# Performance work log

Measured on AMD Instinct MI355X. Metric: run time of the kernel, lower is better.

Reference implementation:

```python
import jax, jax.numpy as jnp
import numpy as np

N = 50000          # total atoms in batch
E = 1_600_000      # total edges (flattened neighbor list)
ELEM = 64          # elem_fea_len
NBR = 32           # nbr_fea_len
EPS = 1e-5         # BatchNorm eps


def _batchnorm(x, gamma, beta):
    # training-mode BatchNorm1d: per-feature batch stats (biased variance)
    mean = x.mean(axis=0)
    var = ((x - mean) ** 2).mean(axis=0)
    return gamma * (x - mean) * jax.lax.rsqrt(var + EPS) + beta


def setup_inputs() -> dict:
    key = jax.random.key(0)
    ks = jax.random.split(key, 6)
    atom_in_fea = jax.random.normal(ks[0], (N, ELEM), jnp.float32)
    nbr_fea = jax.random.normal(ks[1], (E, NBR), jnp.float32)
    self_fea_idx = jnp.sort(jax.random.randint(ks[2], (E,), 0, N))
    nbr_fea_idx = jax.random.randint(ks[3], (E,), 0, N)
    fan_in = 2 * ELEM + NBR
    W = jax.random.normal(ks[4], (fan_in, 2 * ELEM), jnp.float32) * (1.0 / np.sqrt(fan_in))
    b = jnp.zeros((2 * ELEM,), jnp.float32)
    gamma1 = jnp.ones((2 * ELEM,), jnp.float32)
    beta1 = jnp.zeros((2 * ELEM,), jnp.float32)
    gamma2 = jnp.ones((ELEM,), jnp.float32)
    beta2 = jnp.zeros((ELEM,), jnp.float32)
    return {
        "atom_in_fea": atom_in_fea,
        "nbr_fea": nbr_fea,
        "self_fea_idx": self_fea_idx,
        "nbr_fea_idx": nbr_fea_idx,
        "W": W,
        "b": b,
        "gamma1": gamma1,
        "beta1": beta1,
        "gamma2": gamma2,
        "beta2": beta2,
    }


def reference(atom_in_fea, nbr_fea, self_fea_idx, nbr_fea_idx,
              W, b, gamma1, beta1, gamma2, beta2):
    # gather + concat: (E, 2*ELEM + NBR)
    total_fea = jnp.concatenate(
        [atom_in_fea[self_fea_idx], atom_in_fea[nbr_fea_idx], nbr_fea], axis=1)
    total_fea = total_fea @ W + b                    # fc_full: (E, 2*ELEM)
    total_fea = _batchnorm(total_fea, gamma1, beta1)  # bn1
    filter_fea, core_fea = jnp.split(total_fea, 2, axis=1)
    nbr_msg = jax.nn.sigmoid(filter_fea) * jax.nn.softplus(core_fea)  # (E, ELEM)
    nbr_sumed = jax.ops.segment_sum(nbr_msg, self_fea_idx, num_segments=N)
    nbr_sumed = _batchnorm(nbr_sumed, gamma2, beta2)  # bn2
    return jax.nn.softplus(atom_in_fea + nbr_sumed)   # residual + softplus2
```

## Files before the change

kernel.cpp:

```cpp
#include <hip/hip_runtime.h>

#define E_TOT 1600000
#define N_AT  50000

typedef unsigned short u16;
typedef __attribute__((ext_vector_type(8))) __bf16 bf16x8;
typedef __attribute__((ext_vector_type(4))) float f32x4;

__device__ __forceinline__ u16 f2bf(float f) {
    unsigned int u = __float_as_uint(f);
    return (u16)((u + 0x7FFFu + ((u >> 16) & 1u)) >> 16);
}
__device__ __forceinline__ float softplus_f(float x) {
    return fmaxf(x, 0.0f) + __logf(1.0f + __expf(-fabsf(x)));
}
__device__ __forceinline__ bf16x8 cvt8(const float* __restrict__ p) {
    f32x4 a = *(const f32x4*)p;
    f32x4 b = *(const f32x4*)(p + 4);
    bf16x8 r;
    r[0] = (__bf16)a[0]; r[1] = (__bf16)a[1]; r[2] = (__bf16)a[2]; r[3] = (__bf16)a[3];
    r[4] = (__bf16)b[0]; r[5] = (__bf16)b[1]; r[6] = (__bf16)b[2]; r[7] = (__bf16)b[3];
    return r;
}

__global__ __launch_bounds__(256) void k_pre(const float* __restrict__ atom,
                                             u16* __restrict__ ab) {
    int i = blockIdx.x * 256 + threadIdx.x;
    ab[i] = f2bf(atom[i]);
}

__global__ __launch_bounds__(256) void k0_swizzle_w(const float* __restrict__ W,
                                                    u16* __restrict__ wf) {
    int t = blockIdx.x * 256 + threadIdx.x;
    if (t >= 5 * 8 * 64 * 8) return;
    int j = t & 7;
    int lane = (t >> 3) & 63;
    int ct = (t >> 9) & 7;
    int kt = t >> 12;
    int k = kt * 32 + (lane >> 4) * 8 + j;
    int c = ct * 16 + (lane & 15);
    wf[t] = f2bf(W[k * 128 + c]);
}

__device__ __forceinline__ void gemm_tile(const u16* __restrict__ ab,
                                          const float* __restrict__ nbr,
                                          const int* __restrict__ sidx,
                                          const int* __restrict__ nidx,
                                          const u16* __restrict__ wf,
                                          int rb, int lane, f32x4 acc[2][8]) {
    const int mrow = lane & 15, quad = lane >> 4;
    const int r0 = rb + mrow, r1 = r0 + 16;
    const int s0 = sidx[r0], s1 = sidx[r1];
    const int n0 = nidx[r0], n1 = nidx[r1];

    const u16* pa00 = ab + s0 * 64 + quad * 8;
    const u16* pa02 = ab + n0 * 64 + quad * 8;
    const u16* pa10 = ab + s1 * 64 + quad * 8;
    const u16* pa12 = ab + n1 * 64 + quad * 8;

    bf16x8 A0[5], A1[5];
    A0[0] = *(const bf16x8*)pa00;        A1[0] = *(const bf16x8*)pa10;
    A0[1] = *(const bf16x8*)(pa00 + 32); A1[1] = *(const bf16x8*)(pa10 + 32);
    A0[2] = *(const bf16x8*)pa02;        A1[2] = *(const bf16x8*)pa12;
    A0[3] = *(const bf16x8*)(pa02 + 32); A1[3] = *(const bf16x8*)(pa12 + 32);
    A0[4] = cvt8(nbr + r0 * 32 + quad * 8);
    A1[4] = cvt8(nbr + r1 * 32 + quad * 8);

#pragma unroll
    for (int kt = 0; kt < 5; kt++) {
#pragma unroll
        for (int ct = 0; ct < 8; ct++) {
            bf16x8 b = *(const bf16x8*)(wf + ((kt * 8 + ct) * 64 + lane) * 8);
            acc[0][ct] = __builtin_amdgcn_mfma_f32_16x16x32_bf16(A0[kt], b, acc[0][ct], 0, 0, 0);
            acc[1][ct] = __builtin_amdgcn_mfma_f32_16x16x32_bf16(A1[kt], b, acc[1][ct], 0, 0, 0);
        }
    }
}

__global__ __launch_bounds__(256) void k1_stats(const u16* __restrict__ ab,
                                                const float* __restrict__ nbr,
                                                const int* __restrict__ sidx,
                                                const int* __restrict__ nidx,
                                                const u16* __restrict__ wf,
                                                float* __restrict__ statsbuf) {
    const int tx = threadIdx.x, lane = tx & 63, w = tx >> 6;
    const int rb = blockIdx.x * 128 + w * 32;

    f32x4 acc[2][8];
#pragma unroll
    for (int i = 0; i < 2; i++)
#pragma unroll
        for (int j = 0; j < 8; j++) { f32x4 z = {0.f, 0.f, 0.f, 0.f}; acc[i][j] = z; }

    gemm_tile(ab, nbr, sidx, nidx, wf, rb, lane, acc);

    __shared__ float bs[256];
    bs[tx] = 0.0f;
    __syncthreads();

    const int mrow = lane & 15, quad = lane >> 4;
#pragma unroll
    for (int ct = 0; ct < 8; ct++) {
        float s = 0.f, q = 0.f;
#pragma unroll
        for (int rf = 0; rf < 2; rf++)
#pragma unroll
            for (int rg = 0; rg < 4; rg++) {
                float v = acc[rf][ct][rg];
                s += v; q += v * v;
            }
        s += __shfl_xor(s, 16, 64); s += __shfl_xor(s, 32, 64);
        q += __shfl_xor(q, 16, 64); q += __shfl_xor(q, 32, 64);
        if (quad == 0) {
            atomicAdd(&bs[ct * 16 + mrow], s);
            atomicAdd(&bs[128 + ct * 16 + mrow], q);
        }
    }
    __syncthreads();
    statsbuf[blockIdx.x * 256 + tx] = bs[tx];
}

__global__ __launch_bounds__(256) void k2_reduce(const float* __restrict__ statsbuf,
                                                 float* __restrict__ sums1) {
    const int tx = threadIdx.x;
    float s = 0.f;
    for (int b = blockIdx.x; b < 12500; b += gridDim.x)
        s += statsbuf[b * 256 + tx];
    atomicAdd(&sums1[tx], s);
}

__global__ __launch_bounds__(256) void k3_msg(const u16* __restrict__ ab,
                                              const float* __restrict__ nbr,
                                              const int* __restrict__ sidx,
                                              const int* __restrict__ nidx,
                                              const u16* __restrict__ wf,
                                              const float* __restrict__ sums1,
                                              const float* __restrict__ g1,
                                              const float* __restrict__ b1,
                                              float* __restrict__ ns) {
    const int tx = threadIdx.x, lane = tx & 63, w = tx >> 6;
    const int blk = blockIdx.x;
    const int rb = blk * 128 + w * 32;

    f32x4 acc[2][8];
#pragma unroll
    for (int i = 0; i < 2; i++)
#pragma unroll
        for (int j = 0; j < 8; j++) { f32x4 z = {0.f, 0.f, 0.f, 0.f}; acc[i][j] = z; }

    gemm_tile(ab, nbr, sidx, nidx, wf, rb, lane, acc);

    __shared__ float msg[128][66];
    const int mrow = lane & 15, quad = lane >> 4;
    const float invE = 1.0f / (float)E_TOT;

#pragma unroll
    for (int ct = 0; ct < 4; ct++) {
        const int cf = ct * 16 + mrow;
        const int cc = cf + 64;
        float mf = sums1[cf] * invE;
        float vf = sums1[128 + cf] * invE - mf * mf;
        float af = g1[cf] * rsqrtf(vf + 1e-5f);
        float kf = b1[cf] - af * mf;
        float mc = sums1[cc] * invE;
        float vc = sums1[128 + cc] * invE - mc * mc;
        float ac = g1[cc] * rsqrtf(vc + 1e-5f);
        float kc = b1[cc] - ac * mc;
#pragma unroll
        for (int rf = 0; rf < 2; rf++)
#pragma unroll
            for (int rg = 0; rg < 4; rg++) {
                float xf = af * acc[rf][ct][rg] + kf;
                float xc = ac * acc[rf][ct + 4][rg] + kc;
                float sg = 1.0f / (1.0f + __expf(-xf));
                msg[w * 32 + rf * 16 + quad * 4 + rg][cf] = sg * softplus_f(xc);
            }
    }
    __syncthreads();

    const int ebase = blk * 128 + w * 32;
    float accum = 0.f;
    int cur = sidx[ebase];
    for (int i = 0; i < 32; i++) {
        int idx = sidx[ebase + i];
        if (idx != cur) {
            atomicAdd(&ns[cur * 64 + lane], accum);
            accum = 0.f;
            cur = idx;
        }
        accum += msg[w * 32 + i][lane];
    }
    atomicAdd(&ns[cur * 64 + lane], accum);
}

__global__ __launch_bounds__(256) void k4_bn2stats(const float* __restrict__ ns,
                                                   float* __restrict__ sums2) {
    const int tx = threadIdx.x;
    const int col = tx & 63, rg = tx >> 6;
    float s = 0.f, q = 0.f;
    for (int r = blockIdx.x * 4 + rg; r < N_AT; r += 256 * 4) {
        float v = ns[r * 64 + col];
        s += v; q += v * v;
    }
    atomicAdd(&sums2[col], s);
    atomicAdd(&sums2[64 + col], q);
}

__global__ __launch_bounds__(256) void k5_final(const float* __restrict__ atom,
                                                const float* __restrict__ ns,
                                                const float* __restrict__ sums2,
                                                const float* __restrict__ g2,
                                                const float* __restrict__ b2,
                                                float* __restrict__ out) {
    const int i = blockIdx.x * 256 + threadIdx.x;
    const int col = i & 63;
    const float invN = 1.0f / (float)N_AT;
    float mean = sums2[col] * invN;
    float var = sums2[64 + col] * invN - mean * mean;
    float a2 = g2[col] * rsqrtf(var + 1e-5f);
    float c2 = b2[col] - a2 * mean;
    float x = atom[i] + a2 * ns[i] + c2;
    out[i] = softplus_f(x);
}

extern "C" void kernel_launch(void* const* d_in, const int* in_sizes, int n_in,
                              void* d_out, int out_size, void* d_ws, size_t ws_size,
                              hipStream_t stream) {
    const float* atom = (const float*)d_in[0];
    const float* nbr  = (const float*)d_in[1];
    const int* sidx   = (const int*)d_in[2];
    const int* nidx   = (const int*)d_in[3];
    const float* W    = (const float*)d_in[4];
    const float* g1   = (const float*)d_in[6];
    const float* b1   = (const float*)d_in[7];
    const float* g2   = (const float*)d_in[8];
    const float* b2   = (const float*)d_in[9];
    float* out = (float*)d_out;

    char* ws = (char*)d_ws;
    const size_t STAT1_OFF = 0;
    const size_t SUM1_OFF  = STAT1_OFF + (size_t)12500 * 256 * 4;
    const size_t NS_OFF    = SUM1_OFF + 1024;
    const size_t SUM2_OFF  = NS_OFF + (size_t)N_AT * 64 * 4;
    const size_t WF_OFF    = SUM2_OFF + 512;
    const size_t AB_OFF    = WF_OFF + 40960;

    float* statsbuf = (float*)(ws + STAT1_OFF);
    float* sums1    = (float*)(ws + SUM1_OFF);
    float* nsumed   = (float*)(ws + NS_OFF);
    float* sums2    = (float*)(ws + SUM2_OFF);
    u16*   wf       = (u16*)(ws + WF_OFF);
    u16*   ab       = (u16*)(ws + AB_OFF);

    hipMemsetAsync(ws + SUM1_OFF, 0, 1024 + (size_t)N_AT * 64 * 4 + 512, stream);

    k_pre<<<(N_AT * 64) / 256, 256, 0, stream>>>(atom, ab);
    k0_swizzle_w<<<80, 256, 0, stream>>>(W, wf);
    k1_stats<<<E_TOT / 128, 256, 0, stream>>>(ab, nbr, sidx, nidx, wf, statsbuf);
    k2_reduce<<<64, 256, 0, stream>>>(statsbuf, sums1);
    k3_msg<<<E_TOT / 128, 256, 0, stream>>>(ab, nbr, sidx, nidx, wf, sums1, g1, b1, nsumed);
    k4_bn2stats<<<256, 256, 0, stream>>>(nsumed, sums2);
    k5_final<<<(N_AT * 64) / 256, 256, 0, stream>>>(atom, nsumed, sums2, g2, b2, out);
}
```

Measured before the change: 803.6 us.

## Fuse setup kernels, stage weights in LDS, cache bf16 nbr features, double tile rows

```diff
diff --git a/kernel.cpp b/kernel.cpp
--- a/kernel.cpp
+++ b/kernel.cpp
@@ -7,6 +7,14 @@
 typedef __attribute__((ext_vector_type(8))) __bf16 bf16x8;
 typedef __attribute__((ext_vector_type(4))) float f32x4;
 
+#define SUM1_OFF 0
+#define SUM2_OFF 1024
+#define WF_OFF   2048
+#define NS_OFF   43008
+#define AB_OFF   12843008
+#define NBRB_OFF 19243008
+#define WS_FULL  121643008ULL
+
 __device__ __forceinline__ u16 f2bf(float f) {
     unsigned int u = __float_as_uint(f);
     return (u16)((u + 0x7FFFu + ((u >> 16) & 1u)) >> 16);
@@ -14,101 +22,128 @@
 __device__ __forceinline__ float softplus_f(float x) {
     return fmaxf(x, 0.0f) + __logf(1.0f + __expf(-fabsf(x)));
 }
-__device__ __forceinline__ bf16x8 cvt8(const float* __restrict__ p) {
-    f32x4 a = *(const f32x4*)p;
-    f32x4 b = *(const f32x4*)(p + 4);
+__device__ __forceinline__ bf16x8 cvt8v(f32x4 a, f32x4 b) {
     bf16x8 r;
     r[0] = (__bf16)a[0]; r[1] = (__bf16)a[1]; r[2] = (__bf16)a[2]; r[3] = (__bf16)a[3];
     r[4] = (__bf16)b[0]; r[5] = (__bf16)b[1]; r[6] = (__bf16)b[2]; r[7] = (__bf16)b[3];
     return r;
 }
 
-__global__ __launch_bounds__(256) void k_pre(const float* __restrict__ atom,
-                                             u16* __restrict__ ab) {
-    int i = blockIdx.x * 256 + threadIdx.x;
-    ab[i] = f2bf(atom[i]);
-}
-
-__global__ __launch_bounds__(256) void k0_swizzle_w(const float* __restrict__ W,
-                                                    u16* __restrict__ wf) {
-    int t = blockIdx.x * 256 + threadIdx.x;
-    if (t >= 5 * 8 * 64 * 8) return;
-    int j = t & 7;
-    int lane = (t >> 3) & 63;
-    int ct = (t >> 9) & 7;
-    int kt = t >> 12;
-    int k = kt * 32 + (lane >> 4) * 8 + j;
-    int c = ct * 16 + (lane & 15);
-    wf[t] = f2bf(W[k * 128 + c]);
-}
-
-__device__ __forceinline__ void gemm_tile(const u16* __restrict__ ab,
-                                          const float* __restrict__ nbr,
-                                          const int* __restrict__ sidx,
-                                          const int* __restrict__ nidx,
-                                          const u16* __restrict__ wf,
-                                          int rb, int lane, f32x4 acc[2][8]) {
+__global__ __launch_bounds__(256) void k_setup(const float* __restrict__ atom,
+                                               const float* __restrict__ W,
+                                               char* __restrict__ ws) {
+    u16* wf   = (u16*)(ws + WF_OFF);
+    float* ns = (float*)(ws + NS_OFF);
+    u16* ab   = (u16*)(ws + AB_OFF);
+    const int tid = blockIdx.x * 256 + threadIdx.x;
+    const int gsz = gridDim.x * 256;
+
+    for (int i = tid; i < 512; i += gsz) ((float*)ws)[i] = 0.0f;
+
+    f32x4 z = {0.f, 0.f, 0.f, 0.f};
+    for (int i = tid; i < N_AT * 64 / 4; i += gsz) ((f32x4*)ns)[i] = z;
+
+    for (int i = tid; i < N_AT * 64 / 4; i += gsz) {
+        f32x4 v = ((const f32x4*)atom)[i];
+        u16 r[4];
+        r[0] = f2bf(v[0]); r[1] = f2bf(v[1]); r[2] = f2bf(v[2]); r[3] = f2bf(v[3]);
+        *(unsigned long long*)(ab + i * 4) =
+            (unsigned long long)r[0] | ((unsigned long long)r[1] << 16) |
+            ((unsigned long long)r[2] << 32) | ((unsigned long long)r[3] << 48);
+    }
+
+    for (int t = tid; t < 20480; t += gsz) {
+        int j = t & 7, l2 = (t >> 3) & 63, ct = (t >> 9) & 7, kt = t >> 12;
+        int k = kt * 32 + (l2 >> 4) * 8 + j;
+        int c = ct * 16 + (l2 & 15);
+        wf[t] = f2bf(W[k * 128 + c]);
+    }
+}
+
+template<bool CVT>
+__global__ __launch_bounds__(256, 2) void k1_stats(const u16* __restrict__ ab,
+                                                   const float* __restrict__ nbr,
+                                                   u16* __restrict__ nbrb,
+                                                   const int* __restrict__ sidx,
+                                                   const int* __restrict__ nidx,
+                                                   const u16* __restrict__ wf,
+                                                   float* __restrict__ sums1) {
+    __shared__ u16 bsm[20480];
+    __shared__ float bs[256];
+    const int tx = threadIdx.x, lane = tx & 63, w = tx >> 6;
     const int mrow = lane & 15, quad = lane >> 4;
-    const int r0 = rb + mrow, r1 = r0 + 16;
-    const int s0 = sidx[r0], s1 = sidx[r1];
-    const int n0 = nidx[r0], n1 = nidx[r1];
-
-    const u16* pa00 = ab + s0 * 64 + quad * 8;
-    const u16* pa02 = ab + n0 * 64 + quad * 8;
-    const u16* pa10 = ab + s1 * 64 + quad * 8;
-    const u16* pa12 = ab + n1 * 64 + quad * 8;
-
-    bf16x8 A0[5], A1[5];
-    A0[0] = *(const bf16x8*)pa00;        A1[0] = *(const bf16x8*)pa10;
-    A0[1] = *(const bf16x8*)(pa00 + 32); A1[1] = *(const bf16x8*)(pa10 + 32);
-    A0[2] = *(const bf16x8*)pa02;        A1[2] = *(const bf16x8*)pa12;
-    A0[3] = *(const bf16x8*)(pa02 + 32); A1[3] = *(const bf16x8*)(pa12 + 32);
-    A0[4] = cvt8(nbr + r0 * 32 + quad * 8);
-    A1[4] = cvt8(nbr + r1 * 32 + quad * 8);
-
-#pragma unroll
-    for (int kt = 0; kt < 5; kt++) {
-#pragma unroll
-        for (int ct = 0; ct < 8; ct++) {
-            bf16x8 b = *(const bf16x8*)(wf + ((kt * 8 + ct) * 64 + lane) * 8);
-            acc[0][ct] = __builtin_amdgcn_mfma_f32_16x16x32_bf16(A0[kt], b, acc[0][ct], 0, 0, 0);
-            acc[1][ct] = __builtin_amdgcn_mfma_f32_16x16x32_bf16(A1[kt], b, acc[1][ct], 0, 0, 0);
-        }
-    }
-}
-
-__global__ __launch_bounds__(256) void k1_stats(const u16* __restrict__ ab,
-                                                const float* __restrict__ nbr,
-                                                const int* __restrict__ sidx,
-                                                const int* __restrict__ nidx,
-                                                const u16* __restrict__ wf,
-                                                float* __restrict__ statsbuf) {
-    const int tx = threadIdx.x, lane = tx & 63, w = tx >> 6;
-    const int rb = blockIdx.x * 128 + w * 32;
-
-    f32x4 acc[2][8];
-#pragma unroll
-    for (int i = 0; i < 2; i++)
-#pragma unroll
-        for (int j = 0; j < 8; j++) { f32x4 z = {0.f, 0.f, 0.f, 0.f}; acc[i][j] = z; }
-
-    gemm_tile(ab, nbr, sidx, nidx, wf, rb, lane, acc);
-
-    __shared__ float bs[256];
+
+#pragma unroll
+    for (int i = 0; i < 10; i++) {
+        int idx = (i * 256 + tx) * 8;
+        *(bf16x8*)&bsm[idx] = *(const bf16x8*)&wf[idx];
+    }
     bs[tx] = 0.0f;
     __syncthreads();
 
-    const int mrow = lane & 15, quad = lane >> 4;
+    const int RB = blockIdx.x * 256;
+    int rr[2][2];
+    const u16* ps[2][2];
+    const u16* pn[2][2];
+#pragma unroll
+    for (int t = 0; t < 2; t++)
+#pragma unroll
+        for (int rf = 0; rf < 2; rf++) {
+            int r = RB + t * 128 + w * 32 + rf * 16 + mrow;
+            rr[t][rf] = r;
+            ps[t][rf] = ab + sidx[r] * 64 + quad * 8;
+            pn[t][rf] = ab + nidx[r] * 64 + quad * 8;
+        }
+
+    f32x4 acc[2][2][8];
+#pragma unroll
+    for (int t = 0; t < 2; t++)
+#pragma unroll
+        for (int rf = 0; rf < 2; rf++)
+#pragma unroll
+            for (int ct = 0; ct < 8; ct++) {
+                f32x4 z = {0.f, 0.f, 0.f, 0.f};
+                acc[t][rf][ct] = z;
+            }
+
+#pragma unroll
+    for (int kt = 0; kt < 5; kt++) {
+        bf16x8 a[2][2];
+#pragma unroll
+        for (int t = 0; t < 2; t++)
+#pragma unroll
+            for (int rf = 0; rf < 2; rf++) {
+                if (kt < 2)      a[t][rf] = *(const bf16x8*)(ps[t][rf] + kt * 32);
+                else if (kt < 4) a[t][rf] = *(const bf16x8*)(pn[t][rf] + (kt - 2) * 32);
+                else {
+                    const float* p = nbr + rr[t][rf] * 32 + quad * 8;
+                    bf16x8 av = cvt8v(*(const f32x4*)p, *(const f32x4*)(p + 4));
+                    if (CVT) *(bf16x8*)(nbrb + rr[t][rf] * 32 + quad * 8) = av;
+                    a[t][rf] = av;
+                }
+            }
+#pragma unroll
+        for (int ct = 0; ct < 8; ct++) {
+            bf16x8 b = *(const bf16x8*)&bsm[((kt * 8 + ct) * 64 + lane) * 8];
+            acc[0][0][ct] = __builtin_amdgcn_mfma_f32_16x16x32_bf16(a[0][0], b, acc[0][0][ct], 0, 0, 0);
+            acc[0][1][ct] = __builtin_amdgcn_mfma_f32_16x16x32_bf16(a[0][1], b, acc[0][1][ct], 0, 0, 0);
+            acc[1][0][ct] = __builtin_amdgcn_mfma_f32_16x16x32_bf16(a[1][0], b, acc[1][0][ct], 0, 0, 0);
+            acc[1][1][ct] = __builtin_amdgcn_mfma_f32_16x16x32_bf16(a[1][1], b, acc[1][1][ct], 0, 0, 0);
+        }
+    }
+
 #pragma unroll
     for (int ct = 0; ct < 8; ct++) {
         float s = 0.f, q = 0.f;
 #pragma unroll
-        for (int rf = 0; rf < 2; rf++)
-#pragma unroll
-            for (int rg = 0; rg < 4; rg++) {
-                float v = acc[rf][ct][rg];
-                s += v; q += v * v;
-            }
+        for (int t = 0; t < 2; t++)
+#pragma unroll
+            for (int rf = 0; rf < 2; rf++)
+#pragma unroll
+                for (int rg = 0; rg < 4; rg++) {
+                    float v = acc[t][rf][ct][rg];
+                    s += v; q += v * v;
+                }
         s += __shfl_xor(s, 16, 64); s += __shfl_xor(s, 32, 64);
         q += __shfl_xor(q, 16, 64); q += __shfl_xor(q, 32, 64);
         if (quad == 0) {
@@ -117,80 +152,133 @@
         }
     }
     __syncthreads();
-    statsbuf[blockIdx.x * 256 + tx] = bs[tx];
-}
-
-__global__ __launch_bounds__(256) void k2_reduce(const float* __restrict__ statsbuf,
-                                                 float* __restrict__ sums1) {
-    const int tx = threadIdx.x;
-    float s = 0.f;
-    for (int b = blockIdx.x; b < 12500; b += gridDim.x)
-        s += statsbuf[b * 256 + tx];
-    atomicAdd(&sums1[tx], s);
-}
-
-__global__ __launch_bounds__(256) void k3_msg(const u16* __restrict__ ab,
-                                              const float* __restrict__ nbr,
-                                              const int* __restrict__ sidx,
-                                              const int* __restrict__ nidx,
-                                              const u16* __restrict__ wf,
-                                              const float* __restrict__ sums1,
-                                              const float* __restrict__ g1,
-                                              const float* __restrict__ b1,
-                                              float* __restrict__ ns) {
+    atomicAdd(&sums1[tx], bs[tx]);
+}
+
+template<bool NB>
+__global__ __launch_bounds__(256, 2) void k3_msg(const u16* __restrict__ ab,
+                                                 const float* __restrict__ nbr,
+                                                 const u16* __restrict__ nbrb,
+                                                 const int* __restrict__ sidx,
+                                                 const int* __restrict__ nidx,
+                                                 const u16* __restrict__ wf,
+                                                 const float* __restrict__ sums1,
+                                                 const float* __restrict__ g1,
+                                                 const float* __restrict__ b1,
+                                                 float* __restrict__ ns) {
+    __shared__ u16 bsm[20480];
+    __shared__ float msg[4][16 * 66];
     const int tx = threadIdx.x, lane = tx & 63, w = tx >> 6;
-    const int blk = blockIdx.x;
-    const int rb = blk * 128 + w * 32;
-
-    f32x4 acc[2][8];
-#pragma unroll
-    for (int i = 0; i < 2; i++)
-#pragma unroll
-        for (int j = 0; j < 8; j++) { f32x4 z = {0.f, 0.f, 0.f, 0.f}; acc[i][j] = z; }
-
-    gemm_tile(ab, nbr, sidx, nidx, wf, rb, lane, acc);
-
-    __shared__ float msg[128][66];
     const int mrow = lane & 15, quad = lane >> 4;
+
+#pragma unroll
+    for (int i = 0; i < 10; i++) {
+        int idx = (i * 256 + tx) * 8;
+        *(bf16x8*)&bsm[idx] = *(const bf16x8*)&wf[idx];
+    }
+    __syncthreads();
+
     const float invE = 1.0f / (float)E_TOT;
-
+    float af[4], kf[4], ac[4], kc[4];
 #pragma unroll
     for (int ct = 0; ct < 4; ct++) {
-        const int cf = ct * 16 + mrow;
-        const int cc = cf + 64;
+        int cf = ct * 16 + mrow, cc = cf + 64;
         float mf = sums1[cf] * invE;
         float vf = sums1[128 + cf] * invE - mf * mf;
-        float af = g1[cf] * rsqrtf(vf + 1e-5f);
-        float kf = b1[cf] - af * mf;
+        af[ct] = g1[cf] * rsqrtf(vf + 1e-5f);
+        kf[ct] = b1[cf] - af[ct] * mf;
         float mc = sums1[cc] * invE;
         float vc = sums1[128 + cc] * invE - mc * mc;
-        float ac = g1[cc] * rsqrtf(vc + 1e-5f);
-        float kc = b1[cc] - ac * mc;
+        ac[ct] = g1[cc] * rsqrtf(vc + 1e-5f);
+        kc[ct] = b1[cc] - ac[ct] * mc;
+    }
+
+    const int RB = blockIdx.x * 256;
+    int rr[2][2];
+    const u16* ps[2][2];
+    const u16* pn[2][2];
+#pragma unroll
+    for (int t = 0; t < 2; t++)
+#pragma unroll
+        for (int rf = 0; rf < 2; rf++) {
+            int r = RB + t * 128 + w * 32 + rf * 16 + mrow;
+            rr[t][rf] = r;
+            ps[t][rf] = ab + sidx[r] * 64 + quad * 8;
+            pn[t][rf] = ab + nidx[r] * 64 + quad * 8;
+        }
+
+    f32x4 acc[2][2][8];
+#pragma unroll
+    for (int t = 0; t < 2; t++)
 #pragma unroll
         for (int rf = 0; rf < 2; rf++)
 #pragma unroll
-            for (int rg = 0; rg < 4; rg++) {
-                float xf = af * acc[rf][ct][rg] + kf;
-                float xc = ac * acc[rf][ct + 4][rg] + kc;
-                float sg = 1.0f / (1.0f + __expf(-xf));
-                msg[w * 32 + rf * 16 + quad * 4 + rg][cf] = sg * softplus_f(xc);
-            }
-    }
-    __syncthreads();
-
-    const int ebase = blk * 128 + w * 32;
-    float accum = 0.f;
-    int cur = sidx[ebase];
-    for (int i = 0; i < 32; i++) {
-        int idx = sidx[ebase + i];
-        if (idx != cur) {
+            for (int ct = 0; ct < 8; ct++) {
+                f32x4 z = {0.f, 0.f, 0.f, 0.f};
+                acc[t][rf][ct] = z;
+            }
+
+#pragma unroll
+    for (int kt = 0; kt < 5; kt++) {
+        bf16x8 a[2][2];
+#pragma unroll
+        for (int t = 0; t < 2; t++)
+#pragma unroll
+            for (int rf = 0; rf < 2; rf++) {
+                if (kt < 2)      a[t][rf] = *(const bf16x8*)(ps[t][rf] + kt * 32);
+                else if (kt < 4) a[t][rf] = *(const bf16x8*)(pn[t][rf] + (kt - 2) * 32);
+                else {
+                    if (NB) a[t][rf] = *(const bf16x8*)(nbrb + rr[t][rf] * 32 + quad * 8);
+                    else {
+                        const float* p = nbr + rr[t][rf] * 32 + quad * 8;
+                        a[t][rf] = cvt8v(*(const f32x4*)p, *(const f32x4*)(p + 4));
+                    }
+                }
+            }
+#pragma unroll
+        for (int ct = 0; ct < 8; ct++) {
+            bf16x8 b = *(const bf16x8*)&bsm[((kt * 8 + ct) * 64 + lane) * 8];
+            acc[0][0][ct] = __builtin_amdgcn_mfma_f32_16x16x32_bf16(a[0][0], b, acc[0][0][ct], 0, 0, 0);
+            acc[0][1][ct] = __builtin_amdgcn_mfma_f32_16x16x32_bf16(a[0][1], b, acc[0][1][ct], 0, 0, 0);
+            acc[1][0][ct] = __builtin_amdgcn_mfma_f32_16x16x32_bf16(a[1][0], b, acc[1][0][ct], 0, 0, 0);
+            acc[1][1][ct] = __builtin_amdgcn_mfma_f32_16x16x32_bf16(a[1][1], b, acc[1][1][ct], 0, 0, 0);
+        }
+    }
+
+    float* mw = msg[w];
+#pragma unroll
+    for (int t = 0; t < 2; t++) {
+#pragma unroll
+        for (int rf = 0; rf < 2; rf++) {
+#pragma unroll
+            for (int ct = 0; ct < 4; ct++) {
+#pragma unroll
+                for (int rg = 0; rg < 4; rg++) {
+                    float xf = af[ct] * acc[t][rf][ct][rg] + kf[ct];
+                    float xc = ac[ct] * acc[t][rf][ct + 4][rg] + kc[ct];
+                    float sg = 1.0f / (1.0f + __expf(-xf));
+                    mw[(quad * 4 + rg) * 66 + ct * 16 + mrow] = sg * softplus_f(xc);
+                }
+            }
+            const int ebase = RB + t * 128 + w * 32 + rf * 16;
+            float mv[16];
+#pragma unroll
+            for (int i = 0; i < 16; i++) mv[i] = mw[i * 66 + lane];
+            float accum = 0.f;
+            int cur = sidx[ebase];
+#pragma unroll
+            for (int i = 0; i < 16; i++) {
+                int idx = sidx[ebase + i];
+                if (idx != cur) {
+                    atomicAdd(&ns[cur * 64 + lane], accum);
+                    accum = 0.f;
+                    cur = idx;
+                }
+                accum += mv[i];
+            }
             atomicAdd(&ns[cur * 64 + lane], accum);
-            accum = 0.f;
-            cur = idx;
-        }
-        accum += msg[w * 32 + i][lane];
-    }
-    atomicAdd(&ns[cur * 64 + lane], accum);
+        }
+    }
 }
 
 __global__ __launch_bounds__(256) void k4_bn2stats(const float* __restrict__ ns,
@@ -219,8 +307,7 @@
     float var = sums2[64 + col] * invN - mean * mean;
     float a2 = g2[col] * rsqrtf(var + 1e-5f);
     float c2 = b2[col] - a2 * mean;
-    float x = atom[i] + a2 * ns[i] + c2;
-    out[i] = softplus_f(x);
+    out[i] = softplus_f(atom[i] + a2 * ns[i] + c2);
 }
 
 extern "C" void kernel_launch(void* const* d_in, const int* in_sizes, int n_in,
@@ -238,27 +325,23 @@
     float* out = (float*)d_out;
 
     char* ws = (char*)d_ws;
-    const size_t STAT1_OFF = 0;
-    const size_t SUM1_OFF  = STAT1_OFF + (size_t)12500 * 256 * 4;
-    const size_t NS_OFF    = SUM1_OFF + 1024;
-    const size_t SUM2_OFF  = NS_OFF + (size_t)N_AT * 64 * 4;
-    const size_t WF_OFF    = SUM2_OFF + 512;
-    const size_t AB_OFF    = WF_OFF + 40960;
-
-    float* statsbuf = (float*)(ws + STAT1_OFF);
-    float* sums1    = (float*)(ws + SUM1_OFF);
-    float* nsumed   = (float*)(ws + NS_OFF);
-    float* sums2    = (float*)(ws + SUM2_OFF);
-    u16*   wf       = (u16*)(ws + WF_OFF);
-    u16*   ab       = (u16*)(ws + AB_OFF);
-
-    hipMemsetAsync(ws + SUM1_OFF, 0, 1024 + (size_t)N_AT * 64 * 4 + 512, stream);
-
-    k_pre<<<(N_AT * 64) / 256, 256, 0, stream>>>(atom, ab);
-    k0_swizzle_w<<<80, 256, 0, stream>>>(W, wf);
-    k1_stats<<<E_TOT / 128, 256, 0, stream>>>(ab, nbr, sidx, nidx, wf, statsbuf);
-    k2_reduce<<<64, 256, 0, stream>>>(statsbuf, sums1);
-    k3_msg<<<E_TOT / 128, 256, 0, stream>>>(ab, nbr, sidx, nidx, wf, sums1, g1, b1, nsumed);
-    k4_bn2stats<<<256, 256, 0, stream>>>(nsumed, sums2);
-    k5_final<<<(N_AT * 64) / 256, 256, 0, stream>>>(atom, nsumed, sums2, g2, b2, out);
-}
+    float* sums1 = (float*)(ws + SUM1_OFF);
+    float* sums2 = (float*)(ws + SUM2_OFF);
+    u16*   wf    = (u16*)(ws + WF_OFF);
+    float* nsum  = (float*)(ws + NS_OFF);
+    u16*   ab    = (u16*)(ws + AB_OFF);
+    u16*   nbrb  = (u16*)(ws + NBRB_OFF);
+
+    const bool big = ws_size >= (size_t)WS_FULL;
+
+    k_setup<<<1024, 256, 0, stream>>>(atom, W, ws);
+    if (big) {
+        k1_stats<true><<<E_TOT / 256, 256, 0, stream>>>(ab, nbr, nbrb, sidx, nidx, wf, sums1);
+        k3_msg<true><<<E_TOT / 256, 256, 0, stream>>>(ab, nbr, nbrb, sidx, nidx, wf, sums1, g1, b1, nsum);
+    } else {
+        k1_stats<false><<<E_TOT / 256, 256, 0, stream>>>(ab, nbr, nbrb, sidx, nidx, wf, sums1);
+        k3_msg<false><<<E_TOT / 256, 256, 0, stream>>>(ab, nbr, nbrb, sidx, nidx, wf, sums1, g1, b1, nsum);
+    }
+    k4_bn2stats<<<256, 256, 0, stream>>>(nsum, sums2);
+    k5_final<<<(N_AT * 64) / 256, 256, 0, stream>>>(atom, nsum, sums2, g2, b2, out);
+}
```

Measured after the change: 741.6 us. 1.08x faster.
